# Kernel optimization log

Measured on AMD Instinct MI355X. Metric: run time of the kernel, lower is better.

## Reference

```python
import jax, jax.numpy as jnp
import numpy as np

B, N, F = 8, 2048, 256

def setup_inputs() -> dict:
    key = jax.random.key(0)
    ks = jax.random.split(key, 8)
    X = jax.random.normal(ks[0], (B, N, F), dtype=jnp.float32)
    A_geo = jax.random.uniform(ks[1], (N, N), dtype=jnp.float32)
    distance_matrix = jax.random.uniform(ks[2], (N, N), dtype=jnp.float32)
    W_w = jax.random.normal(ks[3], (F, F), dtype=jnp.float32) * 0.05
    W_b = jax.random.normal(ks[4], (F,), dtype=jnp.float32) * 0.05
    a1 = jax.random.normal(ks[5], (F,), dtype=jnp.float32) * 0.05  # attn_fc weight, first half (for h_i)
    a2 = jax.random.normal(ks[6], (F,), dtype=jnp.float32) * 0.05  # attn_fc weight, second half (for h_j)
    attn_b = jax.random.normal(ks[7], (1,), dtype=jnp.float32) * 0.05
    threshold = jnp.ones((1,), dtype=jnp.float32) * 0.3
    return {"X": X, "A_geo": A_geo, "distance_matrix": distance_matrix,
            "W_w": W_w, "W_b": W_b, "a1": a1, "a2": a2,
            "attn_b": attn_b, "threshold": threshold}

def reference(X, A_geo, distance_matrix, W_w, W_b, a1, a2, attn_b, threshold):
    alpha = 0.1  # leaky relu slope
    h = jnp.einsum('bnf,of->bno', X, W_w) + W_b            # (B,N,F)
    # attn_fc(cat(h_i,h_j)) == h_i@a1 + h_j@a2 + b (linear decomposition of concat)
    s1 = jnp.einsum('bnf,f->bn', h, a1)                    # score contribution of h_i
    s2 = jnp.einsum('bnf,f->bn', h, a2)                    # score contribution of h_j
    e = jax.nn.leaky_relu(s1[:, :, None] + s2[:, None, :] + attn_b[0],
                          negative_slope=alpha)            # (B,N,N)
    n = distance_matrix.shape[0]
    idx = jnp.arange(n)
    D = distance_matrix.at[idx, idx].set(1.0)              # fill_diagonal_(1.0)
    e = e + 1.0 / (D + 1e-5)[None, :, :]
    mask = jax.nn.sigmoid(10.0 * (A_geo - threshold[0]))   # (N,N)
    e = e * mask[None, :, :]
    attention = jax.nn.softmax(e, axis=-1)                 # dropout: eval mode (identity)
    h_prime = jnp.einsum('bnm,bmf->bnf', attention, h)
    return h_prime
```

## Files before the change

### kernel.cpp

```cpp
#include <hip/hip_runtime.h>
#include <hip/hip_bf16.h>
#include <math.h>

#define Bsz 8
#define Nn  2048
#define Ff  256
#define KCAP 1024
#define THR 60.0f

typedef short short8 __attribute__((ext_vector_type(8)));
typedef float f32x4  __attribute__((ext_vector_type(4)));
typedef unsigned short u16x4 __attribute__((ext_vector_type(4)));
typedef unsigned short u16x8 __attribute__((ext_vector_type(8)));
typedef unsigned int uint;

static __device__ __forceinline__ unsigned short f2bf(float v) {
    __hip_bfloat16 b = __float2bfloat16(v);
    return *reinterpret_cast<unsigned short*>(&b);
}
static __device__ __forceinline__ float bf2f(unsigned short u) {
    return __uint_as_float((uint)u << 16);
}
static __device__ __forceinline__ float fast_rcp(float x) {
    return __builtin_amdgcn_rcpf(x);
}

__global__ __launch_bounds__(256) void k_h(const float* __restrict__ X,
                                           const float* __restrict__ W,
                                           const float* __restrict__ Wb,
                                           const float* __restrict__ a1,
                                           const float* __restrict__ a2,
                                           unsigned short* __restrict__ h,
                                           float* __restrict__ s1,
                                           float* __restrict__ s2) {
    __shared__ char smem[43008];
    char* w_lds = smem;
    char* x_lds = smem + 32768;
    float (*sred1)[4][16] = (float(*)[4][16])(smem + 40960);
    float (*sred2)[4][16] = (float(*)[4][16])(smem + 40960 + 1024);

    const int tid  = threadIdx.x;
    const int lane = tid & 63;
    const int w    = tid >> 6;
    const int r0   = blockIdx.x * 64;
    const int b    = r0 >> 11;
    const int n0   = r0 & 2047;

    f32x4 acc[4][4];
#pragma unroll
    for (int mt = 0; mt < 4; mt++)
#pragma unroll
        for (int nt = 0; nt < 4; nt++) acc[mt][nt] = (f32x4)0.f;

    for (int kc = 0; kc < 4; kc++) {
        const int f0 = kc * 64;
        __syncthreads();
#pragma unroll
        for (int p = 0; p < 16; p++) {
            int idx = tid + p * 256;
            int o = idx >> 4, fi = idx & 15;
            float4 v = *(const float4*)&W[(size_t)o * Ff + f0 + fi * 4];
            u16x4 pk = {f2bf(v.x), f2bf(v.y), f2bf(v.z), f2bf(v.w)};
            *(u16x4*)(w_lds + ((o * 128 + fi * 8) ^ ((o & 7) << 4))) = pk;
        }
#pragma unroll
        for (int p = 0; p < 4; p++) {
            int idx = tid + p * 256;
            int n = idx >> 4, fi = idx & 15;
            float4 v = *(const float4*)&X[(size_t)(r0 + n) * Ff + f0 + fi * 4];
            u16x4 pk = {f2bf(v.x), f2bf(v.y), f2bf(v.z), f2bf(v.w)};
            *(u16x4*)(x_lds + ((n * 128 + fi * 8) ^ ((n & 7) << 4))) = pk;
        }
        __syncthreads();
#pragma unroll
        for (int kt = 0; kt < 2; kt++) {
            short8 bfr[4];
#pragma unroll
            for (int nt = 0; nt < 4; nt++) {
                int n = nt * 16 + (lane & 15);
                bfr[nt] = *(const short8*)(x_lds + ((n * 128 + kt * 64 + (lane >> 4) * 16) ^ ((n & 7) << 4)));
            }
#pragma unroll
            for (int mt = 0; mt < 4; mt++) {
                int o = w * 64 + mt * 16 + (lane & 15);
                short8 afr = *(const short8*)(w_lds + ((o * 128 + kt * 64 + (lane >> 4) * 16) ^ ((o & 7) << 4)));
#pragma unroll
                for (int nt = 0; nt < 4; nt++)
                    acc[mt][nt] = __builtin_amdgcn_mfma_f32_16x16x32_bf16(afr, bfr[nt], acc[mt][nt], 0, 0, 0);
            }
        }
    }

    __syncthreads();
    float s1p[4] = {0.f, 0.f, 0.f, 0.f};
    float s2p[4] = {0.f, 0.f, 0.f, 0.f};
#pragma unroll
    for (int mt = 0; mt < 4; mt++) {
#pragma unroll
        for (int reg = 0; reg < 4; reg++) {
            int o = w * 64 + mt * 16 + (lane >> 4) * 4 + reg;
            float wb = Wb[o], a1v = a1[o], a2v = a2[o];
#pragma unroll
            for (int nt = 0; nt < 4; nt++) {
                float hv = acc[mt][nt][reg] + wb;
                int nl = nt * 16 + (lane & 15);
                *(unsigned short*)(w_lds + nl * 512 + ((o * 2) ^ ((nl & 7) << 4))) = f2bf(hv);
                s1p[nt] += hv * a1v;
                s2p[nt] += hv * a2v;
            }
        }
    }
#pragma unroll
    for (int nt = 0; nt < 4; nt++) {
        s1p[nt] += __shfl_xor(s1p[nt], 16); s1p[nt] += __shfl_xor(s1p[nt], 32);
        s2p[nt] += __shfl_xor(s2p[nt], 16); s2p[nt] += __shfl_xor(s2p[nt], 32);
    }
    if (lane < 16) {
#pragma unroll
        for (int nt = 0; nt < 4; nt++) { sred1[w][nt][lane] = s1p[nt]; sred2[w][nt][lane] = s2p[nt]; }
    }
    __syncthreads();

#pragma unroll
    for (int p = 0; p < 8; p++) {
        int id = tid + p * 256;
        int nl = id >> 5;
        int c16 = (id & 31) * 16;
        u16x8 v = *(const u16x8*)(w_lds + nl * 512 + (c16 ^ ((nl & 7) << 4)));
        *(u16x8*)&h[((size_t)(b * Nn + n0 + nl)) * Ff + (id & 31) * 8] = v;
    }
    if (tid < 64) {
        int nt = tid >> 4, col = tid & 15;
        s1[b * Nn + n0 + nt * 16 + col] = sred1[0][nt][col] + sred1[1][nt][col] + sred1[2][nt][col] + sred1[3][nt][col];
    } else if (tid < 128) {
        int t2 = tid - 64;
        int nt = t2 >> 4, col = t2 & 15;
        s2[b * Nn + n0 + nt * 16 + col] = sred2[0][nt][col] + sred2[1][nt][col] + sred2[2][nt][col] + sred2[3][nt][col];
    }
}

__global__ __launch_bounds__(512) void k_attn(const unsigned short* __restrict__ h,
                                              const float* __restrict__ s1,
                                              const float* __restrict__ s2,
                                              const float* __restrict__ Ageo,
                                              const float* __restrict__ Dm,
                                              const float* __restrict__ ab_p,
                                              const float* __restrict__ thr_p,
                                              float* __restrict__ out) {
    __shared__ uint  ejs[KCAP];
    __shared__ float emks[KCAP];
    __shared__ float edgs[KCAP];
    __shared__ float red[8];
    __shared__ uint  cptr;

    const int i    = blockIdx.x;
    const int tid  = threadIdx.x;
    const int lane = tid & 63;
    const int w    = tid >> 6;
    const float c10 = 10.0f * thr_p[0];

    if (tid == 0) cptr = 0;
    const int j0 = tid * 4;
    float4 a = *(const float4*)&Ageo[(size_t)i * Nn + j0];
    float4 d = *(const float4*)&Dm[(size_t)i * Nn + j0];
    float av[4] = {a.x, a.y, a.z, a.w};
    float dv[4] = {d.x, d.y, d.z, d.w};
    float mk[4], gg[4];
    float m = 0.0f;
#pragma unroll
    for (int c = 0; c < 4; c++) {
        float dd = (j0 + c == i) ? 1.0f : dv[c];
        float mkv = fast_rcp(1.0f + __expf(c10 - 10.0f * av[c]));
        float g   = mkv * fast_rcp(dd + 1e-5f);
        mk[c] = mkv;
        gg[c] = g;
        m = fmaxf(m, g);
    }
#pragma unroll
    for (int dd = 32; dd; dd >>= 1) m = fmaxf(m, __shfl_xor(m, dd));
    if (lane == 0) red[w] = m;
    __syncthreads();
    float gmax = red[0];
#pragma unroll
    for (int k = 1; k < 8; k++) gmax = fmaxf(gmax, red[k]);
    const float cut = gmax - THR;
#pragma unroll
    for (int c = 0; c < 4; c++) {
        if (gg[c] > cut) {
            uint slot = atomicAdd(&cptr, 1u);
            if (slot < KCAP) {
                ejs[slot]  = (uint)(j0 + c);
                emks[slot] = mk[c];
                edgs[slot] = gg[c] - gmax;
            }
        }
    }
    __syncthreads();
    const int C = min(cptr, (uint)KCAP);

    const int b = w;
    const float s1v = s1[b * Nn + i] + ab_p[0];
    const float* s2b = s2 + b * Nn;

    float4 acc = make_float4(0.f, 0.f, 0.f, 0.f);
    float psum = 0.f;

    uint  jA  = ejs[0];
    float mkA = emks[0];
    float dgA = edgs[0];
    float s2A = s2b[jA];
    ushort4 hvA = *(const ushort4*)&h[((size_t)(b * Nn + jA)) * Ff + lane * 4];

    for (int c = 0; c < C; c++) {
        int cn = (c + 1 < C) ? c + 1 : c;
        uint  jB  = ejs[cn];
        float mkB = emks[cn];
        float dgB = edgs[cn];
        float s2B = s2b[jB];
        ushort4 hvB = *(const ushort4*)&h[((size_t)(b * Nn + jB)) * Ff + lane * 4];
        float s = s1v + s2A;
        s = s > 0.f ? s : 0.1f * s;
        float p = __expf(s * mkA + dgA);
        psum += p;
        acc.x += p * bf2f(hvA.x);
        acc.y += p * bf2f(hvA.y);
        acc.z += p * bf2f(hvA.z);
        acc.w += p * bf2f(hvA.w);
        jA = jB; mkA = mkB; dgA = dgB; s2A = s2B; hvA = hvB;
    }

    float inv = 1.0f / psum;
    *(float4*)&out[((size_t)(b * Nn + i)) * Ff + lane * 4] =
        make_float4(acc.x * inv, acc.y * inv, acc.z * inv, acc.w * inv);
}

extern "C" void kernel_launch(void* const* d_in, const int* in_sizes, int n_in,
                              void* d_out, int out_size, void* d_ws, size_t ws_size,
                              hipStream_t stream) {
    const float* X    = (const float*)d_in[0];
    const float* Ageo = (const float*)d_in[1];
    const float* Dm   = (const float*)d_in[2];
    const float* Ww   = (const float*)d_in[3];
    const float* Wb   = (const float*)d_in[4];
    const float* a1   = (const float*)d_in[5];
    const float* a2   = (const float*)d_in[6];
    const float* ab   = (const float*)d_in[7];
    const float* thr  = (const float*)d_in[8];
    float* out = (float*)d_out;

    char* ws = (char*)d_ws;
    float* s1 = (float*)ws;
    float* s2 = s1 + (size_t)Bsz * Nn;
    unsigned short* h = (unsigned short*)(s2 + (size_t)Bsz * Nn);

    k_h<<<256, 256, 0, stream>>>(X, Ww, Wb, a1, a2, h, s1, s2);
    k_attn<<<Nn, 512, 0, stream>>>(h, s1, s2, Ageo, Dm, ab, thr, out);
}
```

Before: 29.69 us.

## Double the k_h block to 512 threads and prefetch next K-chunk into registers

The h-projection kernel now runs 8 waves per block, each computing 32 output features instead of 64, which halves the accumulator registers per wave. Global loads of W and X for the next K-chunk are issued into registers before the MFMA work on the current chunk, so load latency overlaps with compute. The cost is more register pressure from the prefetch buffers and a wider block-level reduction of s1/s2 across 8 waves. Only the first kernel changes, and the attention kernel likely dominates total time.

```diff
diff --git a/kernel.cpp b/kernel.cpp
--- a/kernel.cpp
+++ b/kernel.cpp
@@ -25,7 +25,7 @@
     return __builtin_amdgcn_rcpf(x);
 }
 
-__global__ __launch_bounds__(256) void k_h(const float* __restrict__ X,
+__global__ __launch_bounds__(512) void k_h(const float* __restrict__ X,
                                            const float* __restrict__ W,
                                            const float* __restrict__ Wb,
                                            const float* __restrict__ a1,
@@ -33,11 +33,11 @@
                                            unsigned short* __restrict__ h,
                                            float* __restrict__ s1,
                                            float* __restrict__ s2) {
-    __shared__ char smem[43008];
+    __shared__ char smem[45056];
     char* w_lds = smem;
     char* x_lds = smem + 32768;
     float (*sred1)[4][16] = (float(*)[4][16])(smem + 40960);
-    float (*sred2)[4][16] = (float(*)[4][16])(smem + 40960 + 1024);
+    float (*sred2)[4][16] = (float(*)[4][16])(smem + 40960 + 2048);
 
     const int tid  = threadIdx.x;
     const int lane = tid & 63;
@@ -46,32 +46,51 @@
     const int b    = r0 >> 11;
     const int n0   = r0 & 2047;
 
-    f32x4 acc[4][4];
-#pragma unroll
-    for (int mt = 0; mt < 4; mt++)
+    f32x4 acc[2][4];
+#pragma unroll
+    for (int mt = 0; mt < 2; mt++)
 #pragma unroll
         for (int nt = 0; nt < 4; nt++) acc[mt][nt] = (f32x4)0.f;
 
+    float4 wv[8], xv[2];
+    auto gload = [&](int kc) {
+        const int f0 = kc * 64;
+#pragma unroll
+        for (int p = 0; p < 8; p++) {
+            int idx = tid + p * 512;
+            int o = idx >> 4, fi = idx & 15;
+            wv[p] = *(const float4*)&W[(size_t)o * Ff + f0 + fi * 4];
+        }
+#pragma unroll
+        for (int p = 0; p < 2; p++) {
+            int idx = tid + p * 512;
+            int n = idx >> 4, fi = idx & 15;
+            xv[p] = *(const float4*)&X[(size_t)(r0 + n) * Ff + f0 + fi * 4];
+        }
+    };
+    auto swrite = [&]() {
+#pragma unroll
+        for (int p = 0; p < 8; p++) {
+            int idx = tid + p * 512;
+            int o = idx >> 4, fi = idx & 15;
+            u16x4 pk = {f2bf(wv[p].x), f2bf(wv[p].y), f2bf(wv[p].z), f2bf(wv[p].w)};
+            *(u16x4*)(w_lds + ((o * 128 + fi * 8) ^ ((o & 7) << 4))) = pk;
+        }
+#pragma unroll
+        for (int p = 0; p < 2; p++) {
+            int idx = tid + p * 512;
+            int n = idx >> 4, fi = idx & 15;
+            u16x4 pk = {f2bf(xv[p].x), f2bf(xv[p].y), f2bf(xv[p].z), f2bf(xv[p].w)};
+            *(u16x4*)(x_lds + ((n * 128 + fi * 8) ^ ((n & 7) << 4))) = pk;
+        }
+    };
+
+    gload(0);
     for (int kc = 0; kc < 4; kc++) {
-        const int f0 = kc * 64;
         __syncthreads();
-#pragma unroll
-        for (int p = 0; p < 16; p++) {
-            int idx = tid + p * 256;
-            int o = idx >> 4, fi = idx & 15;
-            float4 v = *(const float4*)&W[(size_t)o * Ff + f0 + fi * 4];
-            u16x4 pk = {f2bf(v.x), f2bf(v.y), f2bf(v.z), f2bf(v.w)};
-            *(u16x4*)(w_lds + ((o * 128 + fi * 8) ^ ((o & 7) << 4))) = pk;
-        }
-#pragma unroll
-        for (int p = 0; p < 4; p++) {
-            int idx = tid + p * 256;
-            int n = idx >> 4, fi = idx & 15;
-            float4 v = *(const float4*)&X[(size_t)(r0 + n) * Ff + f0 + fi * 4];
-            u16x4 pk = {f2bf(v.x), f2bf(v.y), f2bf(v.z), f2bf(v.w)};
-            *(u16x4*)(x_lds + ((n * 128 + fi * 8) ^ ((n & 7) << 4))) = pk;
-        }
+        swrite();
         __syncthreads();
+        if (kc < 3) gload(kc + 1);
 #pragma unroll
         for (int kt = 0; kt < 2; kt++) {
             short8 bfr[4];
@@ -81,8 +100,8 @@
                 bfr[nt] = *(const short8*)(x_lds + ((n * 128 + kt * 64 + (lane >> 4) * 16) ^ ((n & 7) << 4)));
             }
 #pragma unroll
-            for (int mt = 0; mt < 4; mt++) {
-                int o = w * 64 + mt * 16 + (lane & 15);
+            for (int mt = 0; mt < 2; mt++) {
+                int o = w * 32 + mt * 16 + (lane & 15);
                 short8 afr = *(const short8*)(w_lds + ((o * 128 + kt * 64 + (lane >> 4) * 16) ^ ((o & 7) << 4)));
 #pragma unroll
                 for (int nt = 0; nt < 4; nt++)
@@ -95,10 +114,10 @@
     float s1p[4] = {0.f, 0.f, 0.f, 0.f};
     float s2p[4] = {0.f, 0.f, 0.f, 0.f};
 #pragma unroll
-    for (int mt = 0; mt < 4; mt++) {
+    for (int mt = 0; mt < 2; mt++) {
 #pragma unroll
         for (int reg = 0; reg < 4; reg++) {
-            int o = w * 64 + mt * 16 + (lane >> 4) * 4 + reg;
+            int o = w * 32 + mt * 16 + (lane >> 4) * 4 + reg;
             float wb = Wb[o], a1v = a1[o], a2v = a2[o];
 #pragma unroll
             for (int nt = 0; nt < 4; nt++) {
@@ -122,8 +141,8 @@
     __syncthreads();
 
 #pragma unroll
-    for (int p = 0; p < 8; p++) {
-        int id = tid + p * 256;
+    for (int p = 0; p < 4; p++) {
+        int id = tid + p * 512;
         int nl = id >> 5;
         int c16 = (id & 31) * 16;
         u16x8 v = *(const u16x8*)(w_lds + nl * 512 + (c16 ^ ((nl & 7) << 4)));
@@ -131,11 +150,17 @@
     }
     if (tid < 64) {
         int nt = tid >> 4, col = tid & 15;
-        s1[b * Nn + n0 + nt * 16 + col] = sred1[0][nt][col] + sred1[1][nt][col] + sred1[2][nt][col] + sred1[3][nt][col];
+        float v = 0.f;
+#pragma unroll
+        for (int k = 0; k < 8; k++) v += sred1[k][nt][col];
+        s1[b * Nn + n0 + nt * 16 + col] = v;
     } else if (tid < 128) {
         int t2 = tid - 64;
         int nt = t2 >> 4, col = t2 & 15;
-        s2[b * Nn + n0 + nt * 16 + col] = sred2[0][nt][col] + sred2[1][nt][col] + sred2[2][nt][col] + sred2[3][nt][col];
+        float v = 0.f;
+#pragma unroll
+        for (int k = 0; k < 8; k++) v += sred2[k][nt][col];
+        s2[b * Nn + n0 + nt * 16 + col] = v;
     }
 }
 
@@ -253,6 +278,6 @@
     float* s2 = s1 + (size_t)Bsz * Nn;
     unsigned short* h = (unsigned short*)(s2 + (size_t)Bsz * Nn);
 
-    k_h<<<256, 256, 0, stream>>>(X, Ww, Wb, a1, a2, h, s1, s2);
+    k_h<<<256, 512, 0, stream>>>(X, Ww, Wb, a1, a2, h, s1, s2);
     k_attn<<<Nn, 512, 0, stream>>>(h, s1, s2, Ageo, Dm, ab, thr, out);
 }
```

After: 27.57 us. -7.1%, faster.
